# Kernel tuning notes

Hardware: AMD Instinct MI355X
Metric: run time of the kernel (lower is better)

Reference implementation:

```python
import jax, jax.numpy as jnp
import numpy as np

DIM = 256
D_STATE = 64
D_CONV = 4
EXPAND = 2
D_INNER = EXPAND * DIM  # 512
DT_RANK = (DIM + 15) // 16  # 16
BS, N1, N2 = 4, 64, 64


def setup_inputs() -> dict:
    key = jax.random.key(0)
    ks = jax.random.split(key, 12)
    s = 0.02
    x = jax.random.normal(ks[0], (BS, N1, N2, DIM), jnp.float32)
    W_in = jax.random.normal(ks[1], (2 * D_INNER, DIM), jnp.float32) * s
    conv_w = jax.random.normal(ks[2], (D_INNER, D_CONV), jnp.float32) * s
    conv_b = jax.random.normal(ks[3], (D_INNER,), jnp.float32) * s
    W_x = jax.random.normal(ks[4], (DT_RANK + 2 * D_STATE, D_INNER), jnp.float32) * s
    W_dt = jax.random.normal(ks[5], (D_INNER, DT_RANK), jnp.float32) * s
    b_dt = jax.random.normal(ks[6], (D_INNER,), jnp.float32) * s - 4.0  # softplus -> small dt
    A_log = jnp.log(jnp.broadcast_to(jnp.arange(1, D_STATE + 1, dtype=jnp.float32), (D_INNER, D_STATE)))
    D_param = jnp.ones((D_INNER,), jnp.float32)
    W_out = jax.random.normal(ks[7], (DIM, D_INNER), jnp.float32) * s
    ln1_w = jnp.ones((DIM,), jnp.float32)
    ln1_b = jnp.zeros((DIM,), jnp.float32)
    ln2_w = jnp.ones((DIM,), jnp.float32)
    ln2_b = jnp.zeros((DIM,), jnp.float32)
    return dict(x=x, ln1_w=ln1_w, ln1_b=ln1_b, ln2_w=ln2_w, ln2_b=ln2_b,
                W_in=W_in, conv_w=conv_w, conv_b=conv_b, W_x=W_x,
                W_dt=W_dt, b_dt=b_dt, A_log=A_log, D_param=D_param, W_out=W_out)


def _layernorm(x, w, b, eps=1e-6):
    mu = jnp.mean(x, axis=-1, keepdims=True)
    var = jnp.mean((x - mu) ** 2, axis=-1, keepdims=True)
    return (x - mu) * jax.lax.rsqrt(var + eps) * w + b


def _silu(x):
    return x * jax.nn.sigmoid(x)


def _selective_scan(u, dt, A, B, C, D):
    # u, dt: (Bt, L, di); B, C: (Bt, L, ds); A: (di, ds); D: (di,)
    Bt, L, di = u.shape
    ds = A.shape[1]

    def step(h, inp):
        u_t, dt_t, B_t, C_t = inp  # (Bt,di),(Bt,di),(Bt,ds),(Bt,ds)
        dA = jnp.exp(dt_t[:, :, None] * A)                       # (Bt, di, ds)
        h = dA * h + (dt_t * u_t)[:, :, None] * B_t[:, None, :]  # (Bt, di, ds)
        y_t = jnp.einsum('bds,bs->bd', h, C_t)
        return h, y_t

    h0 = jnp.zeros((Bt, di, ds), u.dtype)
    xs = (u.transpose(1, 0, 2), dt.transpose(1, 0, 2),
          B.transpose(1, 0, 2), C.transpose(1, 0, 2))
    _, ys = jax.lax.scan(step, h0, xs)                           # (L, Bt, di)
    return ys.transpose(1, 0, 2) + u * D


def _mamba(xm, W_in, conv_w, conv_b, W_x, W_dt, b_dt, A_log, D_param, W_out):
    # xm: (Bt, L, d_model)
    xz = jnp.einsum('bld,ed->ble', xm, W_in)       # (Bt, L, 2*di)
    xc, z = jnp.split(xz, 2, axis=-1)
    # depthwise causal conv along L
    xc = xc.transpose(0, 2, 1)                     # (Bt, di, L)
    xc = jax.lax.conv_general_dilated(
        xc, conv_w[:, None, :], window_strides=(1,),
        padding=[(D_CONV - 1, 0)], feature_group_count=D_INNER,
        dimension_numbers=('NCH', 'OIH', 'NCH'))
    xc = _silu(xc + conv_b[None, :, None]).transpose(0, 2, 1)  # (Bt, L, di)
    x_dbl = jnp.einsum('bld,ed->ble', xc, W_x)     # (Bt, L, dt_rank+2*ds)
    dt, Bm, Cm = jnp.split(x_dbl, [DT_RANK, DT_RANK + D_STATE], axis=-1)
    dt = jax.nn.softplus(jnp.einsum('blr,dr->bld', dt, W_dt) + b_dt)  # (Bt, L, di)
    A = -jnp.exp(A_log)                            # (di, ds)
    y = _selective_scan(xc, dt, A, Bm, Cm, D_param)
    y = y * _silu(z)
    return jnp.einsum('bld,od->blo', y, W_out)     # (Bt, L, d_model)


def reference(x, ln1_w, ln1_b, ln2_w, ln2_b, W_in, conv_w, conv_b, W_x,
              W_dt, b_dt, A_log, D_param, W_out):
    bs, n1, n2, d = x.shape
    x_norm = _layernorm(x, ln1_w, ln1_b)
    x1 = x_norm.reshape(bs, n1 * n2, d)                                  # row-major
    x2 = x_norm.transpose(0, 2, 1, 3).reshape(bs, n1 * n2, d)            # column-major
    xm = jnp.concatenate([x1, x2], axis=0)                               # (2*bs, L, d)
    xm = _mamba(xm, W_in, conv_w, conv_b, W_x, W_dt, b_dt, A_log, D_param, W_out)
    y = _layernorm(xm, ln2_w, ln2_b)
    y1, y2 = y[:bs], y[bs:]
    y1 = y1.reshape(bs, n1, n2, d)
    y2 = y2.reshape(bs, n2, n1, d).transpose(0, 2, 1, 3)
    return x + y1 + y2
```

## Files before the change

kernel.cpp:

```cpp
#include <hip/hip_runtime.h>
#include <hip/hip_bf16.h>

typedef unsigned short ushort_t;
typedef unsigned int uint_t;
typedef __attribute__((ext_vector_type(8))) short short8;
typedef __attribute__((ext_vector_type(4))) float f32x4;

#define DIMC 256
#define D_INNER 512
#define D_STATE 64
#define DT_RANK 16
#define LSEQ 4096
#define BS2 8
#define MROWS (BS2*LSEQ)

__device__ __forceinline__ int perm_inv(int p) {
    return (p & 3) | ((p & 0x38) >> 1) | ((p & 4) << 3);
}

__device__ __forceinline__ float b2f(ushort_t u) {
    union { uint_t i; float f; } v; v.i = ((uint_t)u) << 16; return v.f;
}
__device__ __forceinline__ ushort_t f2b(float f) {
    union { float f; uint_t i; } v; v.f = f;
    uint_t r = v.i + 0x7FFFu + ((v.i >> 16) & 1u);
    return (ushort_t)(r >> 16);
}

typedef __attribute__((address_space(1))) const unsigned int gas_u32;
typedef __attribute__((address_space(3))) unsigned int las_u32;
__device__ __forceinline__ void gload16(const void* g, void* l) {
    __builtin_amdgcn_global_load_lds((gas_u32*)g, (las_u32*)l, 16, 0, 0);
}

__device__ __forceinline__ void xcd_remap(int gy, int ybits, int& mblk, int& nblk) {
    int idl = blockIdx.x + gridDim.x * blockIdx.y;
    int xcdc = idl & 7;
    int rest = idl >> 3;
    int y = rest & (gy - 1);
    int xhi = rest >> ybits;
    mblk = (xhi * 8 + xcdc) * 128;
    nblk = y * 128;
}

__global__ void cvtw3(const float* __restrict__ s0, ushort_t* __restrict__ d0,
                      const float* __restrict__ s1, ushort_t* __restrict__ d1,
                      const float* __restrict__ s2, ushort_t* __restrict__ d2) {
    int i = blockIdx.x * 256 + threadIdx.x;
    const int n0 = 1024 * 256, n1 = 144 * 512, n2 = 256 * 512;
    if (i < n0) d0[i] = f2b(s0[i]);
    else if (i < n0 + n1) d1[i - n0] = f2b(s1[i - n0]);
    else if (i < n0 + n1 + n2) d2[i - n0 - n1] = f2b(s2[i - n0 - n1]);
}

__global__ void ln1_build_xm(const float* __restrict__ x,
                             const float* __restrict__ w,
                             const float* __restrict__ bb,
                             ushort_t* __restrict__ xm) {
    int row = blockIdx.x;
    int c = threadIdx.x;
    float v = x[(size_t)row * DIMC + c];
    float s1 = v, s2 = v * v;
    for (int off = 32; off; off >>= 1) {
        s1 += __shfl_xor(s1, off, 64);
        s2 += __shfl_xor(s2, off, 64);
    }
    __shared__ float sa[4], sb[4];
    int widx = c >> 6, lane = c & 63;
    if (lane == 0) { sa[widx] = s1; sb[widx] = s2; }
    __syncthreads();
    s1 = sa[0] + sa[1] + sa[2] + sa[3];
    s2 = sb[0] + sb[1] + sb[2] + sb[3];
    float mu = s1 * (1.0f / 256.0f);
    float var = s2 * (1.0f / 256.0f) - mu * mu;
    float xn = (v - mu) * rsqrtf(var + 1e-6f) * w[c] + bb[c];
    ushort_t o = f2b(xn);
    int b = row >> 12, l = row & 4095, i = l >> 6, j = l & 63;
    xm[((size_t)b * LSEQ + l) * DIMC + c] = o;
    xm[((size_t)(4 + b) * LSEQ + (j * 64 + i)) * DIMC + c] = o;
}

__global__ void __launch_bounds__(256, 4)
gemm128(const ushort_t* __restrict__ A,
        const ushort_t* __restrict__ W,
        ushort_t* __restrict__ C, int M, int N, int K) {
    __shared__ ushort_t Ash[128 * 32];
    __shared__ ushort_t Bsh[128 * 32];
    int tid = threadIdx.x;
    int lane = tid & 63, widx = tid >> 6;
    int wm = widx & 1, wn = widx >> 1;
    int l16 = lane & 15, quad = lane >> 4;
    int mblk, nblk;
    xcd_remap(2, 1, mblk, nblk);
    f32x4 acc[4][4];
    #pragma unroll
    for (int i = 0; i < 4; ++i)
        #pragma unroll
        for (int j = 0; j < 4; ++j)
            acc[i][j] = f32x4{0.0f, 0.0f, 0.0f, 0.0f};
    int srow = tid >> 2;
    int sseg = (tid & 3) * 8;
    bool jv[4];
    #pragma unroll
    for (int j = 0; j < 4; ++j) jv[j] = (nblk + wn * 64 + j * 16) < N;

    for (int k0 = 0; k0 < K; k0 += 32) {
        __syncthreads();
        #pragma unroll
        for (int q = 0; q < 2; ++q) {
            int row = q * 64 + srow;
            gload16(&A[(size_t)(mblk + row) * K + k0 + sseg], &Ash[row * 32 + sseg]);
            gload16(&W[(size_t)(nblk + row) * K + k0 + sseg], &Bsh[row * 32 + sseg]);
        }
        __syncthreads();
        short8 af[4], bf[4];
        #pragma unroll
        for (int i = 0; i < 4; ++i)
            af[i] = *(const short8*)&Ash[(wm * 64 + i * 16 + l16) * 32 + quad * 8];
        #pragma unroll
        for (int j = 0; j < 4; ++j)
            bf[j] = *(const short8*)&Bsh[(wn * 64 + j * 16 + l16) * 32 + quad * 8];
        #pragma unroll
        for (int i = 0; i < 4; ++i)
            #pragma unroll
            for (int j = 0; j < 4; ++j)
                if (jv[j])
                    acc[i][j] = __builtin_amdgcn_mfma_f32_16x16x32_bf16(af[i], bf[j], acc[i][j], 0, 0, 0);
    }
    #pragma unroll
    for (int i = 0; i < 4; ++i) {
        #pragma unroll
        for (int j = 0; j < 4; ++j) {
            if (!jv[j]) continue;
            int col = nblk + wn * 64 + j * 16 + l16;
            #pragma unroll
            for (int r = 0; r < 4; ++r) {
                int row = mblk + wm * 64 + i * 16 + quad * 4 + r;
                C[(size_t)row * N + col] = f2b(acc[i][j][r]);
            }
        }
    }
}

__global__ void __launch_bounds__(256, 4)
gemm128_split(const ushort_t* __restrict__ A,
              const ushort_t* __restrict__ W,
              ushort_t* __restrict__ outX,
              ushort_t* __restrict__ outZ) {
    const int K = 256;
    __shared__ ushort_t Ash[128 * 32];
    __shared__ ushort_t Bsh[128 * 32];
    int tid = threadIdx.x;
    int lane = tid & 63, widx = tid >> 6;
    int wm = widx & 1, wn = widx >> 1;
    int l16 = lane & 15, quad = lane >> 4;
    int mblk, nblk;
    xcd_remap(8, 3, mblk, nblk);
    f32x4 acc[4][4];
    #pragma unroll
    for (int i = 0; i < 4; ++i)
        #pragma unroll
        for (int j = 0; j < 4; ++j)
            acc[i][j] = f32x4{0.0f, 0.0f, 0.0f, 0.0f};
    int srow = tid >> 2;
    int sseg = (tid & 3) * 8;
    for (int k0 = 0; k0 < K; k0 += 32) {
        __syncthreads();
        #pragma unroll
        for (int q = 0; q < 2; ++q) {
            int row = q * 64 + srow;
            gload16(&A[(size_t)(mblk + row) * K + k0 + sseg], &Ash[row * 32 + sseg]);
            gload16(&W[(size_t)(nblk + row) * K + k0 + sseg], &Bsh[row * 32 + sseg]);
        }
        __syncthreads();
        short8 af[4], bf[4];
        #pragma unroll
        for (int i = 0; i < 4; ++i)
            af[i] = *(const short8*)&Ash[(wm * 64 + i * 16 + l16) * 32 + quad * 8];
        #pragma unroll
        for (int j = 0; j < 4; ++j)
            bf[j] = *(const short8*)&Bsh[(wn * 64 + j * 16 + l16) * 32 + quad * 8];
        #pragma unroll
        for (int i = 0; i < 4; ++i)
            #pragma unroll
            for (int j = 0; j < 4; ++j)
                acc[i][j] = __builtin_amdgcn_mfma_f32_16x16x32_bf16(af[i], bf[j], acc[i][j], 0, 0, 0);
    }
    #pragma unroll
    for (int i = 0; i < 4; ++i) {
        #pragma unroll
        for (int j = 0; j < 4; ++j) {
            int colg = nblk + wn * 64 + j * 16 + l16;
            ushort_t* dst = (colg < 512) ? outX : outZ;
            int col = colg & 511;
            #pragma unroll
            for (int r = 0; r < 4; ++r) {
                int row = mblk + wm * 64 + i * 16 + quad * 4 + r;
                dst[(size_t)row * 512 + col] = f2b(acc[i][j][r]);
            }
        }
    }
}

__global__ void conv_silu_t(const ushort_t* __restrict__ xh,
                            const float* __restrict__ cw,
                            const float* __restrict__ cb,
                            ushort_t* __restrict__ xc,
                            ushort_t* __restrict__ u_T) {
    int bt0 = blockIdx.x * 64;
    int d0  = blockIdx.y * 64;
    int b   = bt0 >> 12;
    int t0  = bt0 & 4095;
    __shared__ ushort_t tin[67][66];
    __shared__ ushort_t tout[64][66];
    int tid = threadIdx.x, lane = tid & 63, widx = tid >> 6;
    for (int r = widx; r < 67; r += 4) {
        int tt = t0 - 3 + r;
        tin[r][lane] = (tt >= 0) ? xh[((size_t)bt0 - 3 + r) * 512 + d0 + lane] : (ushort_t)0;
    }
    __syncthreads();
    for (int dd = widx; dd < 64; dd += 4) {
        int d = d0 + dd;
        float acc = cb[d];
        #pragma unroll
        for (int k = 0; k < 4; ++k)
            acc += cw[d * 4 + k] * b2f(tin[lane + k][dd]);
        float s = acc / (1.0f + __expf(-acc));
        ushort_t o = f2b(s);
        u_T[((size_t)b * 512 + d) * 4096 + t0 + lane] = o;
        tout[lane][dd] = o;
    }
    __syncthreads();
    for (int r = widx; r < 64; r += 4)
        xc[((size_t)bt0 + r) * 512 + d0 + lane] = tout[r][lane];
}

__global__ void dt_sp_t(const ushort_t* __restrict__ xdbl,
                        const float* __restrict__ wdt,
                        const float* __restrict__ bdt,
                        const ushort_t* __restrict__ u_T,
                        ushort_t* __restrict__ dt_T,
                        ushort_t* __restrict__ w_T,
                        f32x4* __restrict__ BCfI) {
    int bt0 = blockIdx.x * 64;
    int d0  = blockIdx.y * 64;
    int b   = bt0 >> 12;
    int t0  = bt0 & 4095;
    __shared__ float din[64][17];
    int tid = threadIdx.x;
    for (int i = tid; i < 64 * 16; i += 256) {
        int r = i >> 4, k = i & 15;
        din[r][k] = b2f(xdbl[((size_t)bt0 + r) * 144 + k]);
    }
    __syncthreads();
    int lane = tid & 63, widx = tid >> 6;
    for (int dd = widx; dd < 64; dd += 4) {
        int d = d0 + dd;
        float acc = bdt[d];
        #pragma unroll
        for (int k = 0; k < 16; ++k)
            acc += din[lane][k] * wdt[d * 16 + k];
        float sp = (acc > 20.0f) ? acc : log1pf(__expf(acc));
        size_t idx = ((size_t)b * 512 + d) * 4096 + t0 + lane;
        dt_T[idx] = f2b(sp);
        float uvv = b2f(u_T[idx]);
        w_T[idx] = f2b(sp * uvv);
    }
    if (blockIdx.y == 0) {
        for (int i = tid; i < 32 * 64; i += 256) {
            int p = i >> 6, s = i & 63;
            int sg = perm_inv(s);
            const ushort_t* rpe = xdbl + ((size_t)bt0 + 2 * p) * 144;
            const ushort_t* rpo = rpe + 144;
            f32x4 v;
            v.x = b2f(rpe[16 + sg]); v.y = b2f(rpe[80 + sg]);
            v.z = b2f(rpo[16 + sg]); v.w = b2f(rpo[80 + sg]);
            BCfI[((size_t)(bt0 >> 1) + p) * 64 + s] = v;
        }
    }
}

template<int LVL>
__device__ __forceinline__ float merge_lvl_t(float left, float right, int lane) {
    constexpr int XBIT = (LVL == 0) ? 0 : (LVL == 1) ? 1 : (LVL == 2) ? 3 : 2;
    bool bit = (lane >> XBIT) & 1;
    float send = bit ? left : right;
    float keep = bit ? right : left;
    float recv;
    if constexpr (LVL == 0)
        recv = __int_as_float(__builtin_amdgcn_update_dpp(
            0, __float_as_int(send), 0xB1, 0xF, 0xF, false));
    else if constexpr (LVL == 1)
        recv = __int_as_float(__builtin_amdgcn_update_dpp(
            0, __float_as_int(send), 0x4E, 0xF, 0xF, false));
    else if constexpr (LVL == 2)
        recv = __int_as_float(__builtin_amdgcn_update_dpp(
            0, __float_as_int(send), 0x128, 0xF, 0xF, false));
    else
        recv = __shfl_xor(send, 4, 64);
    return keep + recv;
}
__device__ __forceinline__ float merge16_swap(float a, float b) {
    asm volatile("s_nop 1\n\tv_permlane16_swap_b32 %0, %1" : "+v"(a), "+v"(b));
    return a + b;
}
__device__ __forceinline__ float merge32_swap(float a, float b) {
    asm volatile("s_nop 1\n\tv_permlane32_swap_b32 %0, %1" : "+v"(a), "+v"(b));
    return a + b;
}

__global__ void __launch_bounds__(256, 4)
scan18(const ushort_t* __restrict__ dt_T,
       ushort_t* uT_ysT,
       const ushort_t* __restrict__ w_T,
       const f32x4* __restrict__ BCfI,
       const float* __restrict__ Alog,
       const float* __restrict__ Dp) {
    __shared__ f32x4 BCsh[32][64];
    int tid = threadIdx.x;
    int lane = tid & 63, widx = tid >> 6;
    int wid = blockIdx.x * 4 + widx;
    int b = wid >> 9, d = wid & 511;
    int pinv = perm_inv(lane);
    float a2 = -__expf(Alog[d * 64 + pinv]) * 1.442695041f;
    float Dd = Dp[d];
    float h = 0.0f;
    size_t rowT = ((size_t)b * 512 + d) * 4096;
    uint_t rowTu = __builtin_amdgcn_readfirstlane((uint_t)rowT);
    size_t base = (size_t)b * LSEQ;
    size_t woff = (size_t)widx * 8192 + (size_t)lane * 16;

    {
        const char* gsrc = (const char*)BCfI + base * 512;
        char* ldst = (char*)&BCsh[0][0];
        #pragma unroll
        for (int it = 0; it < 8; ++it)
            gload16(gsrc + woff + (size_t)it * 1024, ldst + woff + (size_t)it * 1024);
    }
    __syncthreads();

    ushort_t ypend = 0;
    #pragma unroll 1
    for (int sl = 0; sl < 64; ++sl) {
        int t0 = sl * 64;
        f32x4 pr0, pr1, pr2, pr3, pr4, pr5, pr6, pr7;
        if (sl < 63) {
            const char* g0 = (const char*)BCfI + (size_t)(base + t0 + 64) * 512 + woff;
            const char* g1 = g0 + 4096;
            asm volatile(
                "global_load_dwordx4 %0, %8, off\n\t"
                "global_load_dwordx4 %1, %8, off offset:1024\n\t"
                "global_load_dwordx4 %2, %8, off offset:2048\n\t"
                "global_load_dwordx4 %3, %8, off offset:3072\n\t"
                "global_load_dwordx4 %4, %9, off\n\t"
                "global_load_dwordx4 %5, %9, off offset:1024\n\t"
                "global_load_dwordx4 %6, %9, off offset:2048\n\t"
                "global_load_dwordx4 %7, %9, off offset:3072"
                : "=&v"(pr0), "=&v"(pr1), "=&v"(pr2), "=&v"(pr3),
                  "=&v"(pr4), "=&v"(pr5), "=&v"(pr6), "=&v"(pr7)
                : "v"(g0), "v"(g1)
                : "memory");
        }
        if (sl) uT_ysT[rowT + t0 - 64 + pinv] = ypend;
        const uint_t* dtw = (const uint_t*)(dt_T + rowTu) + (t0 >> 1);
        const uint_t* wwp = (const uint_t*)(w_T + rowTu) + (t0 >> 1);
        float uv = b2f(uT_ysT[rowT + t0 + pinv]);
        float acc[4], s4, s5, yfin = 0.0f, v16 = 0.0f;
        #pragma unroll 1
        for (int j1 = 0; j1 < 4; ++j1) {
            f32x4 qs[8];
            #pragma unroll
            for (int q = 0; q < 8; ++q)
                qs[q] = BCsh[j1 * 8 + q][lane];
            #pragma unroll
            for (int jj = 0; jj < 16; ++jj) {
                int j = j1 * 16 + jj;
                uint_t pd = dtw[j >> 1];
                uint_t pw = wwp[j >> 1];
                float sdt = __uint_as_float((jj & 1) ? (pd & 0xFFFF0000u) : (pd << 16));
                float sw  = __uint_as_float((jj & 1) ? (pw & 0xFFFF0000u) : (pw << 16));
                float bcx = (jj & 1) ? qs[jj >> 1].z : qs[jj >> 1].x;
                float bcy = (jj & 1) ? qs[jj >> 1].w : qs[jj >> 1].y;
                float dA = __builtin_amdgcn_exp2f(sdt * a2);
                h = dA * h + sw * bcx;
                float v = h * bcy;
                const int dest = (jj == 15) ? 4 : __builtin_ctz(~(unsigned)jj);
                if (0 < dest) v = merge_lvl_t<0>(acc[0], v, lane);
                if (1 < dest) v = merge_lvl_t<1>(acc[1], v, lane);
                if (2 < dest) v = merge_lvl_t<2>(acc[2], v, lane);
                if (3 < dest) v = merge16_swap(acc[3], v);
                if (jj == 15) v16 = v;
                else acc[dest] = v;
            }
            if ((j1 & 1) == 0) {
                s4 = v16;
            } else {
                float m = merge32_swap(s4, v16);
                if (j1 == 1) s5 = m;
                else yfin = merge_lvl_t<5>(s5, m, lane);
            }
        }
        ypend = f2b(yfin + uv * Dd);
        __syncthreads();
        if (sl < 63) {
            asm volatile("s_waitcnt vmcnt(0)" ::: "memory");
            char* ldst = (char*)&BCsh[0][0] + woff;
            *(f32x4*)(ldst + 0)    = pr0;
            *(f32x4*)(ldst + 1024) = pr1;
            *(f32x4*)(ldst + 2048) = pr2;
            *(f32x4*)(ldst + 3072) = pr3;
            *(f32x4*)(ldst + 4096) = pr4;
            *(f32x4*)(ldst + 5120) = pr5;
            *(f32x4*)(ldst + 6144) = pr6;
            *(f32x4*)(ldst + 7168) = pr7;
        }
        __syncthreads();
    }
    uT_ysT[rowT + (LSEQ - 64) + pinv] = ypend;
}

__global__ void gate_t(const ushort_t* __restrict__ ysT,
                       const ushort_t* __restrict__ zb,
                       ushort_t* __restrict__ ys) {
    int bt0 = blockIdx.x * 64;
    int d0  = blockIdx.y * 64;
    int b   = bt0 >> 12;
    int t0  = bt0 & 4095;
    __shared__ ushort_t tile[64][66];
    int tid = threadIdx.x, lane = tid & 63, widx = tid >> 6;
    for (int dd = widx; dd < 64; dd += 4)
        tile[dd][lane] = ysT[((size_t)b * 512 + d0 + dd) * 4096 + t0 + lane];
    __syncthreads();
    for (int r = widx; r < 64; r += 4) {
        float zv = b2f(zb[((size_t)bt0 + r) * 512 + d0 + lane]);
        float yv = b2f(tile[lane][r]);
        float g = zv / (1.0f + __expf(-zv));
        ys[((size_t)bt0 + r) * 512 + d0 + lane] = f2b(yv * g);
    }
}

__global__ void final_ln_add(const ushort_t* __restrict__ outm,
                             const float* __restrict__ x,
                             const float* __restrict__ w,
                             const float* __restrict__ bb,
                             float* __restrict__ out) {
    int row = blockIdx.x;
    int c = threadIdx.x;
    int b = row >> 12, l = row & 4095, i = l >> 6, j = l & 63;
    size_t rA = ((size_t)b * LSEQ + l) * DIMC;
    size_t rB = ((size_t)(4 + b) * LSEQ + (j * 64 + i)) * DIMC;
    float va = b2f(outm[rA + c]);
    float vb = b2f(outm[rB + c]);
    float s1 = va, s2 = va * va, s3 = vb, s4 = vb * vb;
    for (int off = 32; off; off >>= 1) {
        s1 += __shfl_xor(s1, off, 64);
        s2 += __shfl_xor(s2, off, 64);
        s3 += __shfl_xor(s3, off, 64);
        s4 += __shfl_xor(s4, off, 64);
    }
    __shared__ float sm[4][4];
    int widx = c >> 6, lane = c & 63;
    if (lane == 0) { sm[widx][0] = s1; sm[widx][1] = s2; sm[widx][2] = s3; sm[widx][3] = s4; }
    __syncthreads();
    s1 = sm[0][0] + sm[1][0] + sm[2][0] + sm[3][0];
    s2 = sm[0][1] + sm[1][1] + sm[2][1] + sm[3][1];
    s3 = sm[0][2] + sm[1][2] + sm[2][2] + sm[3][2];
    s4 = sm[0][3] + sm[1][3] + sm[2][3] + sm[3][3];
    float muA = s1 * (1.0f / 256.0f), varA = s2 * (1.0f / 256.0f) - muA * muA;
    float muB = s3 * (1.0f / 256.0f), varB = s4 * (1.0f / 256.0f) - muB * muB;
    float lw = w[c], lb = bb[c];
    float ya = (va - muA) * rsqrtf(varA + 1e-6f) * lw + lb;
    float yb = (vb - muB) * rsqrtf(varB + 1e-6f) * lw + lb;
    float xo = x[(size_t)row * DIMC + c];
    out[(size_t)row * DIMC + c] = xo + ya + yb;
}

extern "C" void kernel_launch(void* const* d_in, const int* in_sizes, int n_in,
                              void* d_out, int out_size, void* d_ws, size_t ws_size,
                              hipStream_t stream) {
    const float* x      = (const float*)d_in[0];
    const float* ln1_w  = (const float*)d_in[1];
    const float* ln1_b  = (const float*)d_in[2];
    const float* ln2_w  = (const float*)d_in[3];
    const float* ln2_b  = (const float*)d_in[4];
    const float* W_in   = (const float*)d_in[5];
    const float* conv_w = (const float*)d_in[6];
    const float* conv_b = (const float*)d_in[7];
    const float* W_x    = (const float*)d_in[8];
    const float* W_dt   = (const float*)d_in[9];
    const float* b_dt   = (const float*)d_in[10];
    const float* A_log  = (const float*)d_in[11];
    const float* D_par  = (const float*)d_in[12];
    const float* W_out  = (const float*)d_in[13];
    float* out = (float*)d_out;

    char* ws = (char*)d_ws;
    size_t off = 0;
    ushort_t* wb_in  = (ushort_t*)(ws + off); off += (size_t)1024 * 256 * 2;
    ushort_t* wb_x   = (ushort_t*)(ws + off); off += (size_t)144 * 512 * 2;
    ushort_t* wb_out = (ushort_t*)(ws + off); off += (size_t)256 * 512 * 2;
    const size_t R0 = (size_t)MROWS * DIMC * 2;
    const size_t R1 = (size_t)MROWS * 512 * 2;
    ushort_t* r0 = (ushort_t*)(ws + off); off += R0;
    ushort_t* r1 = (ushort_t*)(ws + off); off += R1;
    ushort_t* r2 = (ushort_t*)(ws + off); off += R1;
    ushort_t* r3 = (ushort_t*)(ws + off); off += R1;
    ushort_t* r4 = (ushort_t*)(ws + off); off += R1;
    f32x4*    BCfI = (f32x4*)(ws + off);  off += (size_t)MROWS * 64 * 8;

    ushort_t* xm    = r0;
    ushort_t* xdbl  = r0;
    ushort_t* outm  = r0;
    ushort_t* xhalf = r1;
    ushort_t* dt_T  = r1;
    ushort_t* zb    = r2;
    ushort_t* xc    = r3;
    ushort_t* w_T   = r3;
    ushort_t* ys    = r3;
    ushort_t* u_T   = r4;

    const int ncvt = 1024 * 256 + 144 * 512 + 256 * 512;
    hipLaunchKernelGGL(cvtw3, dim3((ncvt + 255) / 256), dim3(256), 0, stream,
                       W_in, wb_in, W_x, wb_x, W_out, wb_out);

    hipLaunchKernelGGL(ln1_build_xm, dim3(4 * LSEQ), dim3(256), 0, stream,
                       x, ln1_w, ln1_b, xm);
    hipLaunchKernelGGL(gemm128_split, dim3(MROWS / 128, 8), dim3(256), 0, stream,
                       xm, wb_in, xhalf, zb);
    hipLaunchKernelGGL(conv_silu_t, dim3(MROWS / 64, 8), dim3(256), 0, stream,
                       xhalf, conv_w, conv_b, xc, u_T);
    hipLaunchKernelGGL(gemm128, dim3(MROWS / 128, 2), dim3(256), 0, stream,
                       xc, wb_x, xdbl, MROWS, 144, 512);
    hipLaunchKernelGGL(dt_sp_t, dim3(MROWS / 64, 8), dim3(256), 0, stream,
                       xdbl, W_dt, b_dt, u_T, dt_T, w_T, BCfI);
    hipLaunchKernelGGL(scan18, dim3(BS2 * 512 / 4), dim3(256), 0, stream,
                       dt_T, u_T, w_T, BCfI, A_log, D_par);
    hipLaunchKernelGGL(gate_t, dim3(MROWS / 64, 8), dim3(256), 0, stream,
                       u_T, zb, ys);
    hipLaunchKernelGGL(gemm128, dim3(MROWS / 128, 2), dim3(256), 0, stream,
                       ys, wb_out, outm, MROWS, 256, 512);
    hipLaunchKernelGGL(final_ln_add, dim3(4 * LSEQ), dim3(256), 0, stream,
                       outm, x, ln2_w, ln2_b, out);
}
```

Before: 677.3 us.

## Replace LDS-staged B/C buffering with register double-buffered global loads in scan

The selective-scan kernel no longer stages B/C coefficients through shared memory with two block barriers per 64-step slice. Each wave instead loads its 16-step B/C groups straight from global memory into two alternating register arrays, prefetching the next group while it computes the current one. Blocks are also remapped so that neighbouring block IDs hit different batches, and the final cross-lane reduction order is changed to use permlane32 swaps plus one shuffle. This removes the barriers and LDS traffic, but costs more VGPRs and duplicated global or L2 reads per wave. An unused scan19 variant is left in the file.

```diff
diff --git a/kernel.cpp b/kernel.cpp
--- a/kernel.cpp
+++ b/kernel.cpp
@@ -282,7 +282,7 @@
 
 template<int LVL>
 __device__ __forceinline__ float merge_lvl_t(float left, float right, int lane) {
-    constexpr int XBIT = (LVL == 0) ? 0 : (LVL == 1) ? 1 : (LVL == 2) ? 3 : 2;
+    constexpr int XBIT = (LVL == 0) ? 0 : (LVL == 1) ? 1 : 3;
     bool bit = (lane >> XBIT) & 1;
     float send = bit ? left : right;
     float keep = bit ? right : left;
@@ -293,12 +293,16 @@
     else if constexpr (LVL == 1)
         recv = __int_as_float(__builtin_amdgcn_update_dpp(
             0, __float_as_int(send), 0x4E, 0xF, 0xF, false));
-    else if constexpr (LVL == 2)
+    else
         recv = __int_as_float(__builtin_amdgcn_update_dpp(
             0, __float_as_int(send), 0x128, 0xF, 0xF, false));
-    else
-        recv = __shfl_xor(send, 4, 64);
     return keep + recv;
+}
+__device__ __forceinline__ float merge_x4(float left, float right, int lane) {
+    bool bit = (lane >> 2) & 1;
+    float send = bit ? left : right;
+    float keep = bit ? right : left;
+    return keep + __shfl_xor(send, 4, 64);
 }
 __device__ __forceinline__ float merge16_swap(float a, float b) {
     asm volatile("s_nop 1\n\tv_permlane16_swap_b32 %0, %1" : "+v"(a), "+v"(b));
@@ -309,17 +313,51 @@
     return a + b;
 }
 
+__device__ __forceinline__ void ldgroup(f32x4 (&q)[8], const f32x4* bcrow, int pair0) {
+    #pragma unroll
+    for (int i = 0; i < 8; ++i)
+        q[i] = bcrow[(size_t)(pair0 + i) * 64];
+}
+
+__device__ __forceinline__ float group16(const f32x4 (&qs)[8],
+                                         const uint_t* __restrict__ dtw,
+                                         const uint_t* __restrict__ wwp,
+                                         int dwb, float a2, float& h, int lane) {
+    float acc[4];
+    float v16 = 0.0f;
+    #pragma unroll
+    for (int jj = 0; jj < 16; ++jj) {
+        uint_t pd = dtw[dwb + (jj >> 1)];
+        uint_t pw = wwp[dwb + (jj >> 1)];
+        float sdt = __uint_as_float((jj & 1) ? (pd & 0xFFFF0000u) : (pd << 16));
+        float sw  = __uint_as_float((jj & 1) ? (pw & 0xFFFF0000u) : (pw << 16));
+        float bcx = (jj & 1) ? qs[jj >> 1].z : qs[jj >> 1].x;
+        float bcy = (jj & 1) ? qs[jj >> 1].w : qs[jj >> 1].y;
+        float dA = __builtin_amdgcn_exp2f(sdt * a2);
+        h = dA * h + sw * bcx;
+        float v = h * bcy;
+        const int dest = (jj == 15) ? 4 : __builtin_ctz(~(unsigned)jj);
+        if (0 < dest) v = merge_lvl_t<0>(acc[0], v, lane);
+        if (1 < dest) v = merge_lvl_t<1>(acc[1], v, lane);
+        if (2 < dest) v = merge_lvl_t<2>(acc[2], v, lane);
+        if (3 < dest) v = merge16_swap(acc[3], v);
+        if (jj == 15) v16 = v;
+        else acc[dest] = v;
+    }
+    return v16;
+}
+
 __global__ void __launch_bounds__(256, 4)
-scan18(const ushort_t* __restrict__ dt_T,
+scan19(const ushort_t* __restrict__ dt_T,
        ushort_t* uT_ysT,
        const ushort_t* __restrict__ w_T,
        const f32x4* __restrict__ BCfI,
        const float* __restrict__ Alog,
        const float* __restrict__ Dp) {
-    __shared__ f32x4 BCsh[32][64];
     int tid = threadIdx.x;
     int lane = tid & 63, widx = tid >> 6;
-    int wid = blockIdx.x * 4 + widx;
+    int blk = blockIdx.x;
+    int wid = (blk & 7) * 512 + (blk >> 3) * 4 + widx;
     int b = wid >> 9, d = wid & 511;
     int pinv = perm_inv(lane);
     float a2 = -__expf(Alog[d * 64 + pinv]) * 1.442695041f;
@@ -327,94 +365,80 @@
     float h = 0.0f;
     size_t rowT = ((size_t)b * 512 + d) * 4096;
     uint_t rowTu = __builtin_amdgcn_readfirstlane((uint_t)rowT);
-    size_t base = (size_t)b * LSEQ;
-    size_t woff = (size_t)widx * 8192 + (size_t)lane * 16;
-
-    {
-        const char* gsrc = (const char*)BCfI + base * 512;
-        char* ldst = (char*)&BCsh[0][0];
-        #pragma unroll
-        for (int it = 0; it < 8; ++it)
-            gload16(gsrc + woff + (size_t)it * 1024, ldst + woff + (size_t)it * 1024);
-    }
-    __syncthreads();
-
+    const uint_t* dtw = (const uint_t*)(dt_T + rowTu);
+    const uint_t* wwp = (const uint_t*)(w_T + rowTu);
+    const f32x4* bcrow = BCfI + ((size_t)b * 2048) * 64 + lane;
+
+    f32x4 qA[8], qB[8];
+    ldgroup(qA, bcrow, 0);
     ushort_t ypend = 0;
     #pragma unroll 1
     for (int sl = 0; sl < 64; ++sl) {
         int t0 = sl * 64;
-        f32x4 pr0, pr1, pr2, pr3, pr4, pr5, pr6, pr7;
-        if (sl < 63) {
-            const char* g0 = (const char*)BCfI + (size_t)(base + t0 + 64) * 512 + woff;
-            const char* g1 = g0 + 4096;
-            asm volatile(
-                "global_load_dwordx4 %0, %8, off\n\t"
-                "global_load_dwordx4 %1, %8, off offset:1024\n\t"
-                "global_load_dwordx4 %2, %8, off offset:2048\n\t"
-                "global_load_dwordx4 %3, %8, off offset:3072\n\t"
-                "global_load_dwordx4 %4, %9, off\n\t"
-                "global_load_dwordx4 %5, %9, off offset:1024\n\t"
-                "global_load_dwordx4 %6, %9, off offset:2048\n\t"
-                "global_load_dwordx4 %7, %9, off offset:3072"
-                : "=&v"(pr0), "=&v"(pr1), "=&v"(pr2), "=&v"(pr3),
-                  "=&v"(pr4), "=&v"(pr5), "=&v"(pr6), "=&v"(pr7)
-                : "v"(g0), "v"(g1)
-                : "memory");
-        }
+        int dwb = t0 >> 1;
         if (sl) uT_ysT[rowT + t0 - 64 + pinv] = ypend;
-        const uint_t* dtw = (const uint_t*)(dt_T + rowTu) + (t0 >> 1);
-        const uint_t* wwp = (const uint_t*)(w_T + rowTu) + (t0 >> 1);
         float uv = b2f(uT_ysT[rowT + t0 + pinv]);
-        float acc[4], s4, s5, yfin = 0.0f, v16 = 0.0f;
-        #pragma unroll 1
-        for (int j1 = 0; j1 < 4; ++j1) {
-            f32x4 qs[8];
-            #pragma unroll
-            for (int q = 0; q < 8; ++q)
-                qs[q] = BCsh[j1 * 8 + q][lane];
-            #pragma unroll
-            for (int jj = 0; jj < 16; ++jj) {
-                int j = j1 * 16 + jj;
-                uint_t pd = dtw[j >> 1];
-                uint_t pw = wwp[j >> 1];
-                float sdt = __uint_as_float((jj & 1) ? (pd & 0xFFFF0000u) : (pd << 16));
-                float sw  = __uint_as_float((jj & 1) ? (pw & 0xFFFF0000u) : (pw << 16));
-                float bcx = (jj & 1) ? qs[jj >> 1].z : qs[jj >> 1].x;
-                float bcy = (jj & 1) ? qs[jj >> 1].w : qs[jj >> 1].y;
-                float dA = __builtin_amdgcn_exp2f(sdt * a2);
-                h = dA * h + sw * bcx;
-                float v = h * bcy;
-                const int dest = (jj == 15) ? 4 : __builtin_ctz(~(unsigned)jj);
-                if (0 < dest) v = merge_lvl_t<0>(acc[0], v, lane);
-                if (1 < dest) v = merge_lvl_t<1>(acc[1], v, lane);
-                if (2 < dest) v = merge_lvl_t<2>(acc[2], v, lane);
-                if (3 < dest) v = merge16_swap(acc[3], v);
-                if (jj == 15) v16 = v;
-                else acc[dest] = v;
-            }
-            if ((j1 & 1) == 0) {
-                s4 = v16;
-            } else {
-                float m = merge32_swap(s4, v16);
-                if (j1 == 1) s5 = m;
-                else yfin = merge_lvl_t<5>(s5, m, lane);
-            }
+        float s4, s5, yfin;
+        ldgroup(qB, bcrow, dwb + 8);
+        s4 = group16(qA, dtw, wwp, dwb, a2, h, lane);
+        ldgroup(qA, bcrow, dwb + 16);
+        s5 = merge16_swap(s4, group16(qB, dtw, wwp, dwb + 8, a2, h, lane));
+        ldgroup(qB, bcrow, dwb + 24);
+        s4 = group16(qA, dtw, wwp, dwb + 16, a2, h, lane);
+        if (sl < 63) ldgroup(qA, bcrow, dwb + 32);
+        {
+            float m = merge16_swap(s4, group16(qB, dtw, wwp, dwb + 24, a2, h, lane));
+            float mm = merge32_swap(s5, m);
+            yfin = merge_x4(mm, mm, lane);
         }
         ypend = f2b(yfin + uv * Dd);
-        __syncthreads();
-        if (sl < 63) {
-            asm volatile("s_waitcnt vmcnt(0)" ::: "memory");
-            char* ldst = (char*)&BCsh[0][0] + woff;
-            *(f32x4*)(ldst + 0)    = pr0;
-            *(f32x4*)(ldst + 1024) = pr1;
-            *(f32x4*)(ldst + 2048) = pr2;
-            *(f32x4*)(ldst + 3072) = pr3;
-            *(f32x4*)(ldst + 4096) = pr4;
-            *(f32x4*)(ldst + 5120) = pr5;
-            *(f32x4*)(ldst + 6144) = pr6;
-            *(f32x4*)(ldst + 7168) = pr7;
-        }
-        __syncthreads();
+    }
+    uT_ysT[rowT + (LSEQ - 64) + pinv] = ypend;
+
+    (void)rowTu;
+}
+
+__global__ void __launch_bounds__(256, 4)
+scan19b(const ushort_t* __restrict__ dt_T,
+        ushort_t* uT_ysT,
+        const ushort_t* __restrict__ w_T,
+        const f32x4* __restrict__ BCfI,
+        const float* __restrict__ Alog,
+        const float* __restrict__ Dp) {
+    int tid = threadIdx.x;
+    int lane = tid & 63, widx = tid >> 6;
+    int blk = blockIdx.x;
+    int wid = (blk & 7) * 512 + (blk >> 3) * 4 + widx;
+    int b = wid >> 9, d = wid & 511;
+    int pinv = perm_inv(lane);
+    float a2 = -__expf(Alog[d * 64 + pinv]) * 1.442695041f;
+    float Dd = Dp[d];
+    float h = 0.0f;
+    size_t rowT = ((size_t)b * 512 + d) * 4096;
+    uint_t rowTu = __builtin_amdgcn_readfirstlane((uint_t)rowT);
+    const uint_t* dtw = (const uint_t*)(dt_T + rowTu);
+    const uint_t* wwp = (const uint_t*)(w_T + rowTu);
+    const f32x4* bcrow = BCfI + ((size_t)b * 2048) * 64 + lane;
+
+    f32x4 qA[8], qB[8];
+    ldgroup(qA, bcrow, 0);
+    ushort_t ypend = 0;
+    #pragma unroll 1
+    for (int sl = 0; sl < 64; ++sl) {
+        int t0 = sl * 64;
+        int dwb = t0 >> 1;
+        if (sl) uT_ysT[rowT + t0 - 64 + pinv] = ypend;
+        float uv = b2f(uT_ysT[rowT + t0 + pinv]);
+        ldgroup(qB, bcrow, dwb + 8);
+        float s4 = group16(qA, dtw, wwp, dwb, a2, h, lane);
+        ldgroup(qA, bcrow, dwb + 16);
+        float s5 = merge32_swap(s4, group16(qB, dtw, wwp, dwb + 8, a2, h, lane));
+        ldgroup(qB, bcrow, dwb + 24);
+        s4 = group16(qA, dtw, wwp, dwb + 16, a2, h, lane);
+        if (sl < 63) ldgroup(qA, bcrow, dwb + 32);
+        float m = merge32_swap(s4, group16(qB, dtw, wwp, dwb + 24, a2, h, lane));
+        float yfin = merge_x4(s5, m, lane);
+        ypend = f2b(yfin + uv * Dd);
     }
     uT_ysT[rowT + (LSEQ - 64) + pinv] = ypend;
 }
@@ -533,7 +557,7 @@
                        xc, wb_x, xdbl, MROWS, 144, 512);
     hipLaunchKernelGGL(dt_sp_t, dim3(MROWS / 64, 8), dim3(256), 0, stream,
                        xdbl, W_dt, b_dt, u_T, dt_T, w_T, BCfI);
-    hipLaunchKernelGGL(scan18, dim3(BS2 * 512 / 4), dim3(256), 0, stream,
+    hipLaunchKernelGGL(scan19b, dim3(BS2 * 512 / 4), dim3(256), 0, stream,
                        dt_T, u_T, w_T, BCfI, A_log, D_par);
     hipLaunchKernelGGL(gate_t, dim3(MROWS / 64, 8), dim3(256), 0, stream,
                        u_T, zb, ys);
```

New measurement: 636.6 us. -6.0%, faster.
